# Optimization experiments

Hardware: AMD Instinct MI355X
Metric: run time of the kernel (lower is better)

## Reference

```python
import jax, jax.numpy as jnp
import numpy as np

B, S, DIM = 2, 2048, 2048
NH, NKV, HD = 32, 8, 64
N_REP = NH // NKV


def apply_rope(x, cos, sin):
    # x: (B, H, S, HD); cos/sin: (S, HD//2)
    d = x.shape[-1] // 2
    x1, x2 = x[..., :d], x[..., d:]
    c = cos[None, None, :, :]
    s = sin[None, None, :, :]
    return jnp.concatenate([x1 * c - x2 * s, x2 * c + x1 * s], axis=-1)


def setup_inputs() -> dict:
    key = jax.random.key(0)
    ks = jax.random.split(key, 8)
    x = jax.random.normal(ks[0], (B, S, DIM), dtype=jnp.float32)
    # plausible RoPE tables
    inv_freq = 1.0 / (10000.0 ** (jnp.arange(0, HD, 2, dtype=jnp.float32) / HD))
    t = jnp.arange(S, dtype=jnp.float32)
    freqs = jnp.outer(t, inv_freq)  # (S, HD//2)
    rope_cos = jnp.cos(freqs)
    rope_sin = jnp.sin(freqs)
    doc_ids = jnp.sort(jax.random.randint(ks[1], (B, S), 0, 8, dtype=jnp.int32), axis=-1)
    std = 0.02
    Wq = jax.random.normal(ks[2], (NH * HD, DIM), dtype=jnp.float32) * std
    Wk = jax.random.normal(ks[3], (NKV * HD, DIM), dtype=jnp.float32) * std
    Wv = jax.random.normal(ks[4], (NKV * HD, DIM), dtype=jnp.float32) * std
    Wo = jax.random.normal(ks[5], (DIM, NH * HD), dtype=jnp.float32) * std
    return {"x": x, "rope_cos": rope_cos, "rope_sin": rope_sin,
            "doc_ids": doc_ids, "Wq": Wq, "Wk": Wk, "Wv": Wv, "Wo": Wo}


def reference(x, rope_cos, rope_sin, doc_ids, Wq, Wk, Wv, Wo):
    batch, seq_len, _ = x.shape
    q = (x @ Wq.T).reshape(batch, seq_len, NH, HD).transpose(0, 2, 1, 3)   # (B,NH,S,HD)
    k = (x @ Wk.T).reshape(batch, seq_len, NKV, HD).transpose(0, 2, 1, 3)  # (B,NKV,S,HD)
    v = (x @ Wv.T).reshape(batch, seq_len, NKV, HD).transpose(0, 2, 1, 3)

    q = apply_rope(q, rope_cos, rope_sin)
    k = apply_rope(k, rope_cos, rope_sin)

    # GQA expansion (repeat_interleave on head dim)
    k = jnp.repeat(k, N_REP, axis=1)  # (B,NH,S,HD)
    v = jnp.repeat(v, N_REP, axis=1)

    # block-diagonal causal mask from packed doc ids
    doc_mask = doc_ids[:, :, None] == doc_ids[:, None, :]          # (B,S,S)
    causal = jnp.tril(jnp.ones((seq_len, seq_len), dtype=bool))    # (S,S)
    mask = (doc_mask & causal[None])[:, None, :, :]                # (B,1,S,S)

    scale = 1.0 / jnp.sqrt(jnp.asarray(HD, dtype=q.dtype))
    scores = jnp.einsum("bhqd,bhkd->bhqk", q, k) * scale
    scores = jnp.where(mask, scores, jnp.finfo(scores.dtype).min)
    attn = jax.nn.softmax(scores, axis=-1)
    out = jnp.einsum("bhqk,bhkd->bhqd", attn, v)                   # (B,NH,S,HD)
    out = out.transpose(0, 2, 1, 3).reshape(batch, seq_len, NH * HD)
    return out @ Wo.T
```

## Files before the change

kernel.cpp:

```cpp
#include <hip/hip_runtime.h>
#include <hip/hip_bf16.h>

#define BB   2
#define SEQ  2048
#define DIMD 2048
#define NHH  32
#define NKVV 8
#define HDD  64
#define QKVS 3072

typedef __bf16 bf16x8 __attribute__((ext_vector_type(8)));
typedef float  floatx4  __attribute__((ext_vector_type(4)));
typedef float  floatx16 __attribute__((ext_vector_type(16)));

typedef __attribute__((address_space(1))) const void* gas_ptr;
typedef __attribute__((address_space(3))) void*       las_ptr;

#define MFMA16 __builtin_amdgcn_mfma_f32_16x16x32_bf16
#define MFMA32 __builtin_amdgcn_mfma_f32_32x32x16_bf16
#define CBAR() asm volatile("" ::: "memory")
#define EXP2F(x) __builtin_amdgcn_exp2f(x)

__device__ __forceinline__ unsigned short f2bu(float f) {
    __hip_bfloat16 h = __float2bfloat16(f);
    return *reinterpret_cast<unsigned short*>(&h);
}

#define DPPF(x, ctrl) __int_as_float(__builtin_amdgcn_mov_dpp(__float_as_int(x), (ctrl), 0xF, 0xF, true))
__device__ __forceinline__ float red16_max(float x) {
    x = fmaxf(x, DPPF(x, 0xB1));
    x = fmaxf(x, DPPF(x, 0x4E));
    x = fmaxf(x, DPPF(x, 0x124));
    x = fmaxf(x, DPPF(x, 0x128));
    return x;
}
__device__ __forceinline__ float red16_sum(float x) {
    x += DPPF(x, 0xB1);
    x += DPPF(x, 0x4E);
    x += DPPF(x, 0x124);
    x += DPPF(x, 0x128);
    return x;
}

#define C_X  (8u  * 1024 * 1024)
#define C_WQ (4u  * 1024 * 1024)
#define C_WK (1u  * 1024 * 1024)
#define C_WV (1u  * 1024 * 1024)
#define C_WO (4u  * 1024 * 1024)
__global__ void cvt_all(const float* __restrict__ x,  const float* __restrict__ wq,
                        const float* __restrict__ wk, const float* __restrict__ wv,
                        const float* __restrict__ wo,
                        __hip_bfloat16* __restrict__ xb,
                        __hip_bfloat16* __restrict__ wqkv,
                        __hip_bfloat16* __restrict__ wob)
{
    unsigned i = (blockIdx.x * blockDim.x + threadIdx.x) * 4;
    const float* src; __hip_bfloat16* dst;
    if (i < C_X)                       { src = x  + i;                    dst = xb + i; }
    else if (i < C_X + C_WQ)           { unsigned o = i - C_X;            src = wq + o; dst = wqkv + o; }
    else if (i < C_X + C_WQ + C_WK)    { unsigned o = i - C_X - C_WQ;     src = wk + o; dst = wqkv + C_WQ + o; }
    else if (i < C_X + C_WQ + C_WK + C_WV) { unsigned o = i - C_X - C_WQ - C_WK; src = wv + o; dst = wqkv + C_WQ + C_WK + o; }
    else                               { unsigned o = i - C_X - C_WQ - C_WK - C_WV; if (o >= C_WO) return; src = wo + o; dst = wob + o; }
    float4 v = *reinterpret_cast<const float4*>(src);
    dst[0] = __float2bfloat16(v.x);
    dst[1] = __float2bfloat16(v.y);
    dst[2] = __float2bfloat16(v.z);
    dst[3] = __float2bfloat16(v.w);
}

template <typename OutT, bool ROPE>
__global__ __launch_bounds__(256) void gemm32(
    const __hip_bfloat16* __restrict__ Abf,
    const __hip_bfloat16* __restrict__ Wbf,
    OutT* __restrict__ C,
    int M, int N, int K, int ldc,
    const float* __restrict__ cosb, const float* __restrict__ sinb,
    unsigned short* __restrict__ vT)
{
    const __bf16* A = reinterpret_cast<const __bf16*>(Abf);
    const __bf16* W = reinterpret_cast<const __bf16*>(Wbf);

    __shared__ __bf16 As[128 * 64];
    __shared__ __bf16 Bs[128 * 64];

    int tid  = threadIdx.x;
    int wid  = tid >> 6;
    int lane = tid & 63;
    int l31  = lane & 31;
    int lh   = lane >> 5;
    int wm   = (wid & 1) * 64;
    int wn   = (wid >> 1) * 64;
    int bm   = blockIdx.x * 128;
    int bn   = blockIdx.y * 128;

    const __bf16* aS[4]; const __bf16* wS[4];
    #pragma unroll
    for (int i = 0; i < 4; ++i) {
        int slot = tid + 256 * i;
        int r = slot >> 3;
        int c = (slot & 7) ^ (r & 7);
        aS[i] = A + (size_t)(bm + r) * K + c * 8;
        wS[i] = W + (size_t)(bn + r) * K + c * 8;
    }

    floatx16 acc[2][2] = {};

    for (int k0 = 0; k0 < K; k0 += 64) {
        #pragma unroll
        for (int i = 0; i < 4; ++i)
            __builtin_amdgcn_global_load_lds((gas_ptr)(aS[i] + k0),
                (las_ptr)(As + (tid + 256 * i) * 8), 16, 0, 0);
        #pragma unroll
        for (int i = 0; i < 4; ++i)
            __builtin_amdgcn_global_load_lds((gas_ptr)(wS[i] + k0),
                (las_ptr)(Bs + (tid + 256 * i) * 8), 16, 0, 0);
        __syncthreads();

        #pragma unroll
        for (int s = 0; s < 4; ++s) {
            bf16x8 af[2], bfr[2];
            #pragma unroll
            for (int mt = 0; mt < 2; ++mt) {
                int row = wm + mt * 32 + l31;
                int ch  = (s * 2 + lh) ^ (row & 7);
                af[mt] = *reinterpret_cast<const bf16x8*>(As + row * 64 + ch * 8);
            }
            #pragma unroll
            for (int nt = 0; nt < 2; ++nt) {
                int row = wn + nt * 32 + l31;
                int ch  = (s * 2 + lh) ^ (row & 7);
                bfr[nt] = *reinterpret_cast<const bf16x8*>(Bs + row * 64 + ch * 8);
            }
            #pragma unroll
            for (int mt = 0; mt < 2; ++mt)
                #pragma unroll
                for (int nt = 0; nt < 2; ++nt)
                    acc[mt][nt] = MFMA32(af[mt], bfr[nt], acc[mt][nt], 0, 0, 0);
        }
        __syncthreads();
    }

    const int col0 = bn + wn;
    if constexpr (ROPE) {
        if (col0 >= 2560) {
            int kvh = (col0 - 2560) >> 6;
            int b   = bm >> 11;
            #pragma unroll
            for (int mt = 0; mt < 2; ++mt)
                #pragma unroll
                for (int rq = 0; rq < 4; ++rq) {
                    int s0 = (bm & (SEQ - 1)) + wm + mt * 32 + rq * 8 + lh * 4;
                    #pragma unroll
                    for (int nt = 0; nt < 2; ++nt) {
                        int d = nt * 32 + l31;
                        ushort4 u;
                        u.x = f2bu(acc[mt][nt][rq * 4 + 0]);
                        u.y = f2bu(acc[mt][nt][rq * 4 + 1]);
                        u.z = f2bu(acc[mt][nt][rq * 4 + 2]);
                        u.w = f2bu(acc[mt][nt][rq * 4 + 3]);
                        *reinterpret_cast<ushort4*>(
                            vT + ((size_t)(b * NKVV + kvh) * 64 + d) * SEQ + s0) = u;
                    }
                }
        } else {
            #pragma unroll
            for (int mt = 0; mt < 2; ++mt)
                #pragma unroll
                for (int reg = 0; reg < 16; ++reg) {
                    int row = bm + wm + mt * 32 + (reg & 3) + (reg >> 2) * 8 + lh * 4;
                    int s   = row & (SEQ - 1);
                    float x1 = acc[mt][0][reg], x2 = acc[mt][1][reg];
                    float cf = cosb[s * 32 + l31];
                    float sf = sinb[s * 32 + l31];
                    float o1 = x1 * cf - x2 * sf;
                    float o2 = x2 * cf + x1 * sf;
                    C[(size_t)row * ldc + col0 + l31]      = __float2bfloat16(o1);
                    C[(size_t)row * ldc + col0 + 32 + l31] = __float2bfloat16(o2);
                }
        }
    } else {
        #pragma unroll
        for (int mt = 0; mt < 2; ++mt)
            #pragma unroll
            for (int nt = 0; nt < 2; ++nt)
                #pragma unroll
                for (int reg = 0; reg < 16; ++reg) {
                    int row = bm + wm + mt * 32 + (reg & 3) + (reg >> 2) * 8 + lh * 4;
                    int col = col0 + nt * 32 + l31;
                    if constexpr (sizeof(OutT) == 4)
                        C[(size_t)row * ldc + col] = acc[mt][nt][reg];
                    else
                        C[(size_t)row * ldc + col] = __float2bfloat16(acc[mt][nt][reg]);
                }
    }
}

#define SCL2 0.18033688f
#define MASKV -3e30f

__global__ __launch_bounds__(256) void attn_mfma(
    const __hip_bfloat16* __restrict__ qkv,
    const unsigned short* __restrict__ vT,
    const int* __restrict__ doc,
    __hip_bfloat16* __restrict__ ob)
{
    int qblk = (int)gridDim.x - 1 - (int)blockIdx.x;
    int h    = blockIdx.y;
    int b    = blockIdx.z;
    int kvh  = h >> 2;
    int tid  = threadIdx.x;
    int wv   = tid >> 6;
    int lane = tid & 63;
    int l15  = lane & 15;
    int l4   = lane >> 4;
    int q0   = qblk * 128;
    int qw   = q0 + wv * 32;

    __shared__ unsigned short Ks[2][64 * 64];
    __shared__ unsigned short Vts[2][64 * 64];
    __shared__ int            kdoc[2][64];
    __shared__ unsigned short Pb[4][32][76];

    const unsigned short* qus = reinterpret_cast<const unsigned short*>(qkv);
    const unsigned short* kus = qus + 2048;
    const int* docb = doc + b * SEQ;

    bf16x8 aq[2][2];
    #pragma unroll
    for (int qt = 0; qt < 2; ++qt) {
        const unsigned short* qrow = qus + (size_t)(b * SEQ + qw + qt * 16 + l15) * QKVS + h * HDD;
        aq[qt][0] = *reinterpret_cast<const bf16x8*>(qrow + l4 * 8);
        aq[qt][1] = *reinterpret_cast<const bf16x8*>(qrow + 32 + l4 * 8);
    }
    int qd[2][4];
    #pragma unroll
    for (int qt = 0; qt < 2; ++qt)
        #pragma unroll
        for (int r = 0; r < 4; ++r)
            qd[qt][r] = docb[qw + qt * 16 + l4 * 4 + r];
    int qd_w   = docb[qw];
    int qd_w31 = docb[qw + 31];
    int qd_blk = docb[q0];
    bool qdu   = (qd_w == qd_w31);

    float mrow[2][4], lrow[2][4];
    #pragma unroll
    for (int qt = 0; qt < 2; ++qt)
        #pragma unroll
        for (int r = 0; r < 4; ++r) { mrow[qt][r] = -1e30f; lrow[qt][r] = 0.f; }
    floatx4 accO[2][4] = {};

    int slot0 = tid, slot1 = tid + 256;
    int row0 = slot0 >> 3, g0 = (slot0 & 7) ^ (row0 & 7);
    int row1 = slot1 >> 3, g1 = (slot1 & 7) ^ (row1 & 7);
    const unsigned short* vtb = vT + ((size_t)(b * NKVV + kvh) * 64) * SEQ;

    int kc_end = 2 * qblk + 1;
    unsigned mask;
    {
        bool v = false;
        if (lane <= kc_end && lane < 32)
            v = (docb[lane * 64 + 63] >= qd_blk);
        mask = (unsigned)__ballot(v);
    }

    auto stagec = [&](int buf, int kc) {
        int k0 = kc * 64;
        __builtin_amdgcn_global_load_lds(
            (gas_ptr)(kus + (size_t)(b * SEQ + k0 + row0) * QKVS + kvh * HDD + g0 * 8),
            (las_ptr)(&Ks[buf][slot0 * 8]), 16, 0, 0);
        __builtin_amdgcn_global_load_lds(
            (gas_ptr)(kus + (size_t)(b * SEQ + k0 + row1) * QKVS + kvh * HDD + g1 * 8),
            (las_ptr)(&Ks[buf][slot1 * 8]), 16, 0, 0);
        __builtin_amdgcn_global_load_lds(
            (gas_ptr)(vtb + (size_t)row0 * SEQ + k0 + g0 * 8),
            (las_ptr)(&Vts[buf][slot0 * 8]), 16, 0, 0);
        __builtin_amdgcn_global_load_lds(
            (gas_ptr)(vtb + (size_t)row1 * SEQ + k0 + g1 * 8),
            (las_ptr)(&Vts[buf][slot1 * 8]), 16, 0, 0);
        __builtin_amdgcn_global_load_lds(
            (gas_ptr)(docb + k0 + lane),
            (las_ptr)(&kdoc[buf][lane]), 4, 0, 0);
    };

    int p  = 0;
    int kc = (int)__builtin_ctz(mask);
    mask &= mask - 1;
    stagec(0, kc);

    while (true) {
        int nkc = -1;
        if (mask) {
            nkc = (int)__builtin_ctz(mask);
            mask &= mask - 1;
            stagec(p ^ 1, nkc);
            asm volatile("s_waitcnt vmcnt(5)" ::: "memory");
        } else {
            asm volatile("s_waitcnt vmcnt(0)" ::: "memory");
        }
        CBAR(); __builtin_amdgcn_s_barrier(); CBAR();

        int k0 = kc * 64;
        int kd_first = kdoc[p][0];
        int kd_last  = kdoc[p][63];
        if (k0 <= qw + 31 && kd_last >= qd_w) {
            bool full = qdu && (kd_first == kd_last) && (kd_last == qd_w)
                        && (k0 + 64 <= qw);

            bf16x8 bk[4][2];
            #pragma unroll
            for (int t = 0; t < 4; ++t) {
                int krow = t * 16 + l15;
                bk[t][0] = *reinterpret_cast<const bf16x8*>(&Ks[p][krow * 64 + ((l4 ^ (krow & 7)) * 8)]);
                bk[t][1] = *reinterpret_cast<const bf16x8*>(&Ks[p][krow * 64 + (((l4 + 4) ^ (krow & 7)) * 8)]);
            }

            #pragma unroll
            for (int qt = 0; qt < 2; ++qt) {
                float s[4][4];
                #pragma unroll
                for (int t = 0; t < 4; ++t) {
                    floatx4 a = {};
                    a = MFMA16(aq[qt][0], bk[t][0], a, 0, 0, 0);
                    a = MFMA16(aq[qt][1], bk[t][1], a, 0, 0, 0);
                    if (full) {
                        #pragma unroll
                        for (int r = 0; r < 4; ++r) s[t][r] = a[r] * SCL2;
                    } else {
                        int key = k0 + t * 16 + l15;
                        int kd  = kdoc[p][t * 16 + l15];
                        #pragma unroll
                        for (int r = 0; r < 4; ++r) {
                            int qrow = qw + qt * 16 + l4 * 4 + r;
                            bool valid = (kd == qd[qt][r]) && (key <= qrow);
                            s[t][r] = valid ? a[r] * SCL2 : MASKV;
                        }
                    }
                }
                #pragma unroll
                for (int r = 0; r < 4; ++r) {
                    float pm = fmaxf(fmaxf(s[0][r], s[1][r]), fmaxf(s[2][r], s[3][r]));
                    pm = red16_max(pm);
                    float mnew = fmaxf(mrow[qt][r], pm);
                    float alpha = EXP2F(mrow[qt][r] - mnew);
                    mrow[qt][r] = mnew;
                    float ps = 0.f;
                    #pragma unroll
                    for (int t = 0; t < 4; ++t) {
                        float pv = EXP2F(s[t][r] - mnew);
                        Pb[wv][qt * 16 + l4 * 4 + r][t * 16 + l15] = f2bu(pv);
                        ps += pv;
                    }
                    ps = red16_sum(ps);
                    lrow[qt][r] = lrow[qt][r] * alpha + ps;
                    #pragma unroll
                    for (int t = 0; t < 4; ++t) accO[qt][t][r] *= alpha;
                }
            }

            bf16x8 bvf[4][2];
            #pragma unroll
            for (int t = 0; t < 4; ++t) {
                int vrow = t * 16 + l15;
                bvf[t][0] = *reinterpret_cast<const bf16x8*>(&Vts[p][vrow * 64 + ((l4 ^ (vrow & 7)) * 8)]);
                bvf[t][1] = *reinterpret_cast<const bf16x8*>(&Vts[p][vrow * 64 + (((l4 + 4) ^ (vrow & 7)) * 8)]);
            }
            #pragma unroll
            for (int qt = 0; qt < 2; ++qt) {
                bf16x8 ap0 = *reinterpret_cast<const bf16x8*>(&Pb[wv][qt * 16 + l15][l4 * 8]);
                bf16x8 ap1 = *reinterpret_cast<const bf16x8*>(&Pb[wv][qt * 16 + l15][32 + l4 * 8]);
                #pragma unroll
                for (int t = 0; t < 4; ++t) {
                    accO[qt][t] = MFMA16(ap0, bvf[t][0], accO[qt][t], 0, 0, 0);
                    accO[qt][t] = MFMA16(ap1, bvf[t][1], accO[qt][t], 0, 0, 0);
                }
            }
        }
        CBAR(); __builtin_amdgcn_s_barrier(); CBAR();
        if (nkc < 0) break;
        kc = nkc; p ^= 1;
    }

    #pragma unroll
    for (int qt = 0; qt < 2; ++qt)
        #pragma unroll
        for (int r = 0; r < 4; ++r) {
            float inv = 1.0f / lrow[qt][r];
            size_t base = (size_t)(b * SEQ + qw + qt * 16 + l4 * 4 + r) * (NHH * HDD) + h * HDD;
            #pragma unroll
            for (int t = 0; t < 4; ++t)
                ob[base + t * 16 + l15] = __float2bfloat16(accO[qt][t][r] * inv);
        }
}

extern "C" void kernel_launch(void* const* d_in, const int* in_sizes, int n_in,
                              void* d_out, int out_size, void* d_ws, size_t ws_size,
                              hipStream_t stream) {
    const float* x  = (const float*)d_in[0];
    const float* rc = (const float*)d_in[1];
    const float* rs = (const float*)d_in[2];
    const int*   dc = (const int*)d_in[3];
    const float* Wq = (const float*)d_in[4];
    const float* Wk = (const float*)d_in[5];
    const float* Wv = (const float*)d_in[6];
    const float* Wo = (const float*)d_in[7];
    float* out = (float*)d_out;

    const int M    = BB * SEQ;
    const int KVD  = NKVV * HDD;
    const int QKVN = DIMD + 2 * KVD;

    char* ws = (char*)d_ws;
    size_t off = 0;
    auto alloc = [&](size_t elems) { __hip_bfloat16* p = (__hip_bfloat16*)(ws + off); off += elems * 2; return p; };
    __hip_bfloat16* xb   = alloc((size_t)M * DIMD);
    __hip_bfloat16* wqkv = alloc((size_t)QKVN * DIMD);
    __hip_bfloat16* wob  = alloc((size_t)DIMD * DIMD);
    __hip_bfloat16* qkv  = alloc((size_t)M * QKVN);
    __hip_bfloat16* abuf = alloc((size_t)M * DIMD);
    unsigned short* vtb  = (unsigned short*)alloc((size_t)BB * NKVV * HDD * SEQ);

    {
        unsigned total4 = (C_X + C_WQ + C_WK + C_WV + C_WO) / 4;
        cvt_all<<<dim3((total4 + 255) / 256), 256, 0, stream>>>(
            x, Wq, Wk, Wv, Wo, xb, wqkv, wob);
    }

    gemm32<__hip_bfloat16, true><<<dim3(M / 128, QKVN / 128), 256, 0, stream>>>(
        xb, wqkv, qkv, M, QKVN, DIMD, QKVN, rc, rs, vtb);

    attn_mfma<<<dim3(SEQ / 128, NHH, BB), 256, 0, stream>>>(qkv, vtb, dc, abuf);

    gemm32<float, false><<<dim3(M / 128, DIMD / 128), 256, 0, stream>>>(
        abuf, wob, out, M, DIMD, DIMD, DIMD, nullptr, nullptr, nullptr);
}
```

Measured before the change: 257.7 us.

## Process two query heads per attention block to reuse staged K/V tiles

Each attention workgroup now handles two query heads that share the same KV head, so every K/V tile staged into LDS feeds twice the MFMA work. The grid's head dimension is halved and per-thread Q fragments, softmax state and output accumulators are doubled. This is meant to halve global-to-LDS K/V traffic and barrier overhead per unit of compute. In exchange it raises register pressure, which may lower occupancy, and cuts the number of workgroups available to spread across CUs.

```diff
diff --git a/kernel.cpp b/kernel.cpp
--- a/kernel.cpp
+++ b/kernel.cpp
@@ -205,9 +205,9 @@
     __hip_bfloat16* __restrict__ ob)
 {
     int qblk = (int)gridDim.x - 1 - (int)blockIdx.x;
-    int h    = blockIdx.y;
+    int h0   = blockIdx.y * 2;
     int b    = blockIdx.z;
-    int kvh  = h >> 2;
+    int kvh  = h0 >> 2;
     int tid  = threadIdx.x;
     int wv   = tid >> 6;
     int lane = tid & 63;
@@ -225,13 +225,15 @@
     const unsigned short* kus = qus + 2048;
     const int* docb = doc + b * SEQ;
 
-    bf16x8 aq[2][2];
+    bf16x8 aq[2][2][2];
     #pragma unroll
-    for (int qt = 0; qt < 2; ++qt) {
-        const unsigned short* qrow = qus + (size_t)(b * SEQ + qw + qt * 16 + l15) * QKVS + h * HDD;
-        aq[qt][0] = *reinterpret_cast<const bf16x8*>(qrow + l4 * 8);
-        aq[qt][1] = *reinterpret_cast<const bf16x8*>(qrow + 32 + l4 * 8);
-    }
+    for (int hd = 0; hd < 2; ++hd)
+        #pragma unroll
+        for (int qt = 0; qt < 2; ++qt) {
+            const unsigned short* qrow = qus + (size_t)(b * SEQ + qw + qt * 16 + l15) * QKVS + (h0 + hd) * HDD;
+            aq[hd][qt][0] = *reinterpret_cast<const bf16x8*>(qrow + l4 * 8);
+            aq[hd][qt][1] = *reinterpret_cast<const bf16x8*>(qrow + 32 + l4 * 8);
+        }
     int qd[2][4];
     #pragma unroll
     for (int qt = 0; qt < 2; ++qt)
@@ -243,12 +245,14 @@
     int qd_blk = docb[q0];
     bool qdu   = (qd_w == qd_w31);
 
-    float mrow[2][4], lrow[2][4];
+    float mrow[2][2][4], lrow[2][2][4];
     #pragma unroll
-    for (int qt = 0; qt < 2; ++qt)
-        #pragma unroll
-        for (int r = 0; r < 4; ++r) { mrow[qt][r] = -1e30f; lrow[qt][r] = 0.f; }
-    floatx4 accO[2][4] = {};
+    for (int hd = 0; hd < 2; ++hd)
+        #pragma unroll
+        for (int qt = 0; qt < 2; ++qt)
+            #pragma unroll
+            for (int r = 0; r < 4; ++r) { mrow[hd][qt][r] = -1e30f; lrow[hd][qt][r] = 0.f; }
+    floatx4 accO[2][2][4] = {};
 
     int slot0 = tid, slot1 = tid + 256;
     int row0 = slot0 >> 3, g0 = (slot0 & 7) ^ (row0 & 7);
@@ -307,72 +311,69 @@
             bool full = qdu && (kd_first == kd_last) && (kd_last == qd_w)
                         && (k0 + 64 <= qw);
 
-            bf16x8 bk[4][2];
+            bf16x8 bk[4][2], bvf[4][2];
             #pragma unroll
             for (int t = 0; t < 4; ++t) {
                 int krow = t * 16 + l15;
-                bk[t][0] = *reinterpret_cast<const bf16x8*>(&Ks[p][krow * 64 + ((l4 ^ (krow & 7)) * 8)]);
-                bk[t][1] = *reinterpret_cast<const bf16x8*>(&Ks[p][krow * 64 + (((l4 + 4) ^ (krow & 7)) * 8)]);
+                bk[t][0]  = *reinterpret_cast<const bf16x8*>(&Ks[p][krow * 64 + ((l4 ^ (krow & 7)) * 8)]);
+                bk[t][1]  = *reinterpret_cast<const bf16x8*>(&Ks[p][krow * 64 + (((l4 + 4) ^ (krow & 7)) * 8)]);
+                bvf[t][0] = *reinterpret_cast<const bf16x8*>(&Vts[p][krow * 64 + ((l4 ^ (krow & 7)) * 8)]);
+                bvf[t][1] = *reinterpret_cast<const bf16x8*>(&Vts[p][krow * 64 + (((l4 + 4) ^ (krow & 7)) * 8)]);
             }
 
             #pragma unroll
-            for (int qt = 0; qt < 2; ++qt) {
-                float s[4][4];
-                #pragma unroll
-                for (int t = 0; t < 4; ++t) {
-                    floatx4 a = {};
-                    a = MFMA16(aq[qt][0], bk[t][0], a, 0, 0, 0);
-                    a = MFMA16(aq[qt][1], bk[t][1], a, 0, 0, 0);
-                    if (full) {
-                        #pragma unroll
-                        for (int r = 0; r < 4; ++r) s[t][r] = a[r] * SCL2;
-                    } else {
-                        int key = k0 + t * 16 + l15;
-                        int kd  = kdoc[p][t * 16 + l15];
-                        #pragma unroll
-                        for (int r = 0; r < 4; ++r) {
-                            int qrow = qw + qt * 16 + l4 * 4 + r;
-                            bool valid = (kd == qd[qt][r]) && (key <= qrow);
-                            s[t][r] = valid ? a[r] * SCL2 : MASKV;
+            for (int hd = 0; hd < 2; ++hd) {
+                #pragma unroll
+                for (int qt = 0; qt < 2; ++qt) {
+                    float s[4][4];
+                    #pragma unroll
+                    for (int t = 0; t < 4; ++t) {
+                        floatx4 a = {};
+                        a = MFMA16(aq[hd][qt][0], bk[t][0], a, 0, 0, 0);
+                        a = MFMA16(aq[hd][qt][1], bk[t][1], a, 0, 0, 0);
+                        if (full) {
+                            #pragma unroll
+                            for (int r = 0; r < 4; ++r) s[t][r] = a[r] * SCL2;
+                        } else {
+                            int key = k0 + t * 16 + l15;
+                            int kd  = kdoc[p][t * 16 + l15];
+                            #pragma unroll
+                            for (int r = 0; r < 4; ++r) {
+                                int qrow = qw + qt * 16 + l4 * 4 + r;
+                                bool valid = (kd == qd[qt][r]) && (key <= qrow);
+                                s[t][r] = valid ? a[r] * SCL2 : MASKV;
+                            }
                         }
                     }
+                    #pragma unroll
+                    for (int r = 0; r < 4; ++r) {
+                        float pm = fmaxf(fmaxf(s[0][r], s[1][r]), fmaxf(s[2][r], s[3][r]));
+                        pm = red16_max(pm);
+                        float mnew = fmaxf(mrow[hd][qt][r], pm);
+                        float alpha = EXP2F(mrow[hd][qt][r] - mnew);
+                        mrow[hd][qt][r] = mnew;
+                        float ps = 0.f;
+                        #pragma unroll
+                        for (int t = 0; t < 4; ++t) {
+                            float pv = EXP2F(s[t][r] - mnew);
+                            Pb[wv][qt * 16 + l4 * 4 + r][t * 16 + l15] = f2bu(pv);
+                            ps += pv;
+                        }
+                        ps = red16_sum(ps);
+                        lrow[hd][qt][r] = lrow[hd][qt][r] * alpha + ps;
+                        #pragma unroll
+                        for (int t = 0; t < 4; ++t) accO[hd][qt][t][r] *= alpha;
+                    }
                 }
                 #pragma unroll
-                for (int r = 0; r < 4; ++r) {
-                    float pm = fmaxf(fmaxf(s[0][r], s[1][r]), fmaxf(s[2][r], s[3][r]));
-                    pm = red16_max(pm);
-                    float mnew = fmaxf(mrow[qt][r], pm);
-                    float alpha = EXP2F(mrow[qt][r] - mnew);
-                    mrow[qt][r] = mnew;
-                    float ps = 0.f;
+                for (int qt = 0; qt < 2; ++qt) {
+                    bf16x8 ap0 = *reinterpret_cast<const bf16x8*>(&Pb[wv][qt * 16 + l15][l4 * 8]);
+                    bf16x8 ap1 = *reinterpret_cast<const bf16x8*>(&Pb[wv][qt * 16 + l15][32 + l4 * 8]);
                     #pragma unroll
                     for (int t = 0; t < 4; ++t) {
-                        float pv = EXP2F(s[t][r] - mnew);
-                        Pb[wv][qt * 16 + l4 * 4 + r][t * 16 + l15] = f2bu(pv);
-                        ps += pv;
+                        accO[hd][qt][t] = MFMA16(ap0, bvf[t][0], accO[hd][qt][t], 0, 0, 0);
+                        accO[hd][qt][t] = MFMA16(ap1, bvf[t][1], accO[hd][qt][t], 0, 0, 0);
                     }
-                    ps = red16_sum(ps);
-                    lrow[qt][r] = lrow[qt][r] * alpha + ps;
-                    #pragma unroll
-                    for (int t = 0; t < 4; ++t) accO[qt][t][r] *= alpha;
-                }
-            }
-
-            bf16x8 bvf[4][2];
-            #pragma unroll
-            for (int t = 0; t < 4; ++t) {
-                int vrow = t * 16 + l15;
-                bvf[t][0] = *reinterpret_cast<const bf16x8*>(&Vts[p][vrow * 64 + ((l4 ^ (vrow & 7)) * 8)]);
-                bvf[t][1] = *reinterpret_cast<const bf16x8*>(&Vts[p][vrow * 64 + (((l4 + 4) ^ (vrow & 7)) * 8)]);
-            }
-            #pragma unroll
-            for (int qt = 0; qt < 2; ++qt) {
-                bf16x8 ap0 = *reinterpret_cast<const bf16x8*>(&Pb[wv][qt * 16 + l15][l4 * 8]);
-                bf16x8 ap1 = *reinterpret_cast<const bf16x8*>(&Pb[wv][qt * 16 + l15][32 + l4 * 8]);
-                #pragma unroll
-                for (int t = 0; t < 4; ++t) {
-                    accO[qt][t] = MFMA16(ap0, bvf[t][0], accO[qt][t], 0, 0, 0);
-                    accO[qt][t] = MFMA16(ap1, bvf[t][1], accO[qt][t], 0, 0, 0);
                 }
             }
         }
@@ -382,15 +383,17 @@
     }
 
     #pragma unroll
-    for (int qt = 0; qt < 2; ++qt)
-        #pragma unroll
-        for (int r = 0; r < 4; ++r) {
-            float inv = 1.0f / lrow[qt][r];
-            size_t base = (size_t)(b * SEQ + qw + qt * 16 + l4 * 4 + r) * (NHH * HDD) + h * HDD;
-            #pragma unroll
-            for (int t = 0; t < 4; ++t)
-                ob[base + t * 16 + l15] = __float2bfloat16(accO[qt][t][r] * inv);
-        }
+    for (int hd = 0; hd < 2; ++hd)
+        #pragma unroll
+        for (int qt = 0; qt < 2; ++qt)
+            #pragma unroll
+            for (int r = 0; r < 4; ++r) {
+                float inv = 1.0f / lrow[hd][qt][r];
+                size_t base = (size_t)(b * SEQ + qw + qt * 16 + l4 * 4 + r) * (NHH * HDD) + (h0 + hd) * HDD;
+                #pragma unroll
+                for (int t = 0; t < 4; ++t)
+                    ob[base + t * 16 + l15] = __float2bfloat16(accO[hd][qt][t][r] * inv);
+            }
 }
 
 extern "C" void kernel_launch(void* const* d_in, const int* in_sizes, int n_in,
@@ -429,7 +432,7 @@
     gemm32<__hip_bfloat16, true><<<dim3(M / 128, QKVN / 128), 256, 0, stream>>>(
         xb, wqkv, qkv, M, QKVN, DIMD, QKVN, rc, rs, vtb);
 
-    attn_mfma<<<dim3(SEQ / 128, NHH, BB), 256, 0, stream>>>(qkv, vtb, dc, abuf);
+    attn_mfma<<<dim3(SEQ / 128, NHH / 2, BB), 256, 0, stream>>>(qkv, vtb, dc, abuf);
 
     gemm32<float, false><<<dim3(M / 128, DIMD / 128), 256, 0, stream>>>(
         abuf, wob, out, M, DIMD, DIMD, DIMD, nullptr, nullptr, nullptr);
```

Result: slower. 275.5 us (+6.9%).
